# Kernel tuning notes

Hardware: AMD Instinct MI355X
Metric: run time of the kernel (lower is better)

The kernel has to match this reference:

```python
import jax, jax.numpy as jnp
import numpy as np

H = 1024
F = 132

def _lstm_cell(x, h, c, Wih, Whh, bih, bhh):
    # PyTorch LSTMCell: gates ordered i, f, g, o
    gates = x @ Wih.T + bih + h @ Whh.T + bhh  # [B, 4H]
    i, f, g, o = jnp.split(gates, 4, axis=-1)
    i = jax.nn.sigmoid(i)
    f = jax.nn.sigmoid(f)
    g = jnp.tanh(g)
    o = jax.nn.sigmoid(o)
    c_new = f * c + i * g
    h_new = o * jnp.tanh(c_new)
    return h_new, c_new


def setup_inputs() -> dict:
    key = jax.random.key(0)
    ks = jax.random.split(key, 16)
    s = 0.02
    return {
        "initial_seq": jax.random.normal(ks[0], (32, 64, F), dtype=jnp.float32),
        "generate_frames_number": 128,
        "W_ih1": jax.random.normal(ks[1], (4 * H, F), dtype=jnp.float32) * s,
        "W_hh1": jax.random.normal(ks[2], (4 * H, H), dtype=jnp.float32) * s,
        "b_ih1": jax.random.normal(ks[3], (4 * H,), dtype=jnp.float32) * s,
        "b_hh1": jax.random.normal(ks[4], (4 * H,), dtype=jnp.float32) * s,
        "W_ih2": jax.random.normal(ks[5], (4 * H, H), dtype=jnp.float32) * s,
        "W_hh2": jax.random.normal(ks[6], (4 * H, H), dtype=jnp.float32) * s,
        "b_ih2": jax.random.normal(ks[7], (4 * H,), dtype=jnp.float32) * s,
        "b_hh2": jax.random.normal(ks[8], (4 * H,), dtype=jnp.float32) * s,
        "W_ih3": jax.random.normal(ks[9], (4 * H, H), dtype=jnp.float32) * s,
        "W_hh3": jax.random.normal(ks[10], (4 * H, H), dtype=jnp.float32) * s,
        "b_ih3": jax.random.normal(ks[11], (4 * H,), dtype=jnp.float32) * s,
        "b_hh3": jax.random.normal(ks[12], (4 * H,), dtype=jnp.float32) * s,
        "W_dec": jax.random.normal(ks[13], (F, H), dtype=jnp.float32) * s,
        "b_dec": jax.random.normal(ks[14], (F,), dtype=jnp.float32) * s,
    }


def reference(initial_seq, generate_frames_number,
              W_ih1, W_hh1, b_ih1, b_hh1,
              W_ih2, W_hh2, b_ih2, b_hh2,
              W_ih3, W_hh3, b_ih3, b_hh3,
              W_dec, b_dec):
    B = initial_seq.shape[0]
    dt = initial_seq.dtype
    zeros = jnp.zeros((B, H), dtype=dt)
    state0 = (zeros, zeros, zeros, zeros, zeros, zeros)  # h0,h1,h2,c0,c1,c2

    def step(state, in_frame):
        h0, h1, h2, c0, c1, c2 = state
        h0, c0 = _lstm_cell(in_frame, h0, c0, W_ih1, W_hh1, b_ih1, b_hh1)
        h1, c1 = _lstm_cell(h0, h1, c1, W_ih2, W_hh2, b_ih2, b_hh2)
        h2, c2 = _lstm_cell(h1, h2, c2, W_ih3, W_hh3, b_ih3, b_hh3)
        out_frame = h2 @ W_dec.T + b_dec  # [B, F]
        return (h0, h1, h2, c0, c1, c2), out_frame

    # Priming pass over the conditioning sequence (outputs discarded except last)
    def prime_step(carry, in_frame):
        state, _ = carry
        state, out = step(state, in_frame)
        return (state, out), None

    init_frame = jnp.zeros((B, F), dtype=dt)
    xs = jnp.swapaxes(initial_seq, 0, 1)  # [T, B, F]
    (state, cur_frame), _ = jax.lax.scan(prime_step, (state0, init_frame), xs)

    def gen_step(carry, _):
        state, frame = carry
        state, out = step(state, frame)
        return (state, out), out

    _, outs = jax.lax.scan(gen_step, (state, cur_frame), None,
                           length=generate_frames_number)  # [N, B, F]
    return jnp.swapaxes(outs, 0, 1)  # [B, N, F]
```

## Files before the change

### kernel.cpp

```cpp
#include <hip/hip_runtime.h>
#include <stdint.h>

typedef unsigned short u16;
typedef unsigned long long u64;
typedef __attribute__((ext_vector_type(8))) short short8;
typedef __attribute__((ext_vector_type(4))) float f32x4;

#define SZ_BIGW    (4096ull*1024ull*2ull)
#define OFF_WHH1   (0ull)
#define OFF_WIH2   (OFF_WHH1 + SZ_BIGW)
#define OFF_WHH2   (OFF_WIH2 + SZ_BIGW)
#define OFF_WIH3   (OFF_WHH2 + SZ_BIGW)
#define OFF_WHH3   (OFF_WIH3 + SZ_BIGW)
#define OFF_MCOMB  (OFF_WHH3 + SZ_BIGW)
#define OFF_WIH1   (OFF_MCOMB + SZ_BIGW)
#define SZ_WIH1    (4096ull*160ull*2ull)
#define OFF_WDECF  (OFF_WIH1 + SZ_WIH1)
#define SZ_WDECF   (160ull*1024ull*2ull)
#define OFF_WDECB  (OFF_WDECF + SZ_WDECF)
#define SZ_WDECB   (1024ull*160ull*2ull)
#define OFF_XPRIM  (OFF_WDECB + SZ_WDECB)
#define SZ_XPRIM   (64ull*5120ull*2ull)
#define OFF_H2HIST (OFF_XPRIM + SZ_XPRIM)
#define SZ_HSLOT   (32768ull*2ull)
#define SZ_H2HIST  (129ull*SZ_HSLOT)
#define OFF_H0R    (OFF_H2HIST + SZ_H2HIST)
#define SZ_HR      (192ull*SZ_HSLOT)
#define OFF_H1R    (OFF_H0R + SZ_HR)
#define OFF_H2R    (OFF_H1R + SZ_HR)
#define SZ_H2R     (64ull*SZ_HSLOT)
#define OFF_ZEROH  (OFF_H2R + SZ_H2R)
#define OFF_FLAGS  (OFF_ZEROH + SZ_HSLOT)
#define SZ_FLAGS   (4096ull)
#define OFF_BS1    (OFF_FLAGS + SZ_FLAGS)
#define OFF_BS1G   (OFF_BS1 + 16384ull)
#define OFF_BS2    (OFF_BS1G + 16384ull)
#define OFF_BS3    (OFF_BS2 + 16384ull)
#define BLOB_SIZE  (OFF_BS3 + 16384ull)

__device__ unsigned char g_blob[BLOB_SIZE];

#define ZERO_BYTES (SZ_HSLOT + SZ_FLAGS)

__device__ __forceinline__ u16 f2bf(float f) {
  unsigned u = __float_as_uint(f);
  u += 0x7fffu + ((u >> 16) & 1u);
  return (u16)(u >> 16);
}
__device__ __forceinline__ float sigm(float x) { return 1.f / (1.f + __expf(-x)); }
__device__ __forceinline__ float tanh_(float x) {
  x = fminf(fmaxf(x, -40.f), 40.f);
  float e = __expf(2.f * x);
  return (e - 1.f) / (e + 1.f);
}

__global__ __launch_bounds__(256) void k_zero(uint4* p, int n) {
  int i = blockIdx.x * 256 + threadIdx.x;
  for (; i < n; i += gridDim.x * 256) p[i] = make_uint4(0u, 0u, 0u, 0u);
}

__global__ __launch_bounds__(256) void k_swizzle(const float* __restrict__ src, u16* __restrict__ dst,
                                                 int J, int Jsrc, int Kpad, int Ksrc, int srcld,
                                                 int transposed, int perm) {
  int total = J * Kpad;
  int nkc = Kpad >> 3;
  for (int o = blockIdx.x * 256 + threadIdx.x; o < total; o += gridDim.x * 256) {
    int chunk = o >> 7, within = o & 127;
    int nt = chunk / nkc, kc = chunk - nt * nkc;
    int jr = within >> 3, ke = within & 7;
    int j = perm ? ((jr >> 2) * 1024 + nt * 4 + (jr & 3)) : (nt * 16 + jr);
    int k = kc * 8 + ke;
    float v = 0.f;
    if (j < Jsrc && k < Ksrc)
      v = transposed ? src[(size_t)k * srcld + j] : src[(size_t)j * srcld + k];
    dst[o] = f2bf(v);
  }
}

__global__ __launch_bounds__(256) void k_xprim(const float* __restrict__ iseq, u16* __restrict__ dst) {
  int o = blockIdx.x * 256 + threadIdx.x;
  if (o >= 64 * 5120) return;
  int t = o / 5120, rem = o - t * 5120;
  int kc = rem >> 8, b = (rem >> 3) & 31, ke = rem & 7;
  int k = kc * 8 + ke;
  float v = (k < 132) ? iseq[(size_t)b * (64 * 132) + t * 132 + k] : 0.f;
  dst[o] = f2bf(v);
}

__global__ __launch_bounds__(256) void k_bias(const float* bih1, const float* bhh1,
                                              const float* bih2, const float* bhh2,
                                              const float* bih3, const float* bhh3,
                                              const float* __restrict__ Wih1, const float* __restrict__ bdec,
                                              float* bs1, float* bs1g, float* bs2, float* bs3) {
  int j = blockIdx.x * 256 + threadIdx.x;
  if (j >= 4096) return;
  float s1 = bih1[j] + bhh1[j];
  float bc = 0.f;
  const float* wr = Wih1 + (size_t)j * 132;
  for (int f = 0; f < 132; ++f) bc += wr[f] * bdec[f];
  bs1[j] = s1;
  bs1g[j] = s1 + bc;
  bs2[j] = bih2[j] + bhh2[j];
  bs3[j] = bih3[j] + bhh3[j];
}

__global__ __launch_bounds__(256) void k_mcomb(const u16* __restrict__ A, const u16* __restrict__ Bm,
                                               u16* __restrict__ dst) {
  int blk = blockIdx.x;
  int mt = blk & 255, jg = blk >> 8;
  int w = threadIdx.x >> 6, l = threadIdx.x & 63, q = l >> 4, r = l & 15;
  int nt = jg * 4 + w;
  f32x4 acc = {};
  for (int ks = 0; ks < 5; ++ks) {
    short8 a = *(const short8*)(A + ((size_t)mt * 20 + ks * 4 + q) * 128 + r * 8);
    short8 b = *(const short8*)(Bm + ((size_t)nt * 20 + ks * 4 + q) * 128 + r * 8);
    acc = __builtin_amdgcn_mfma_f32_16x16x32_bf16(a, b, acc, 0, 0, 0);
  }
  int kout = nt * 16 + r;
#pragma unroll
  for (int i = 0; i < 4; ++i) {
    int jrow = q * 4 + i;
    dst[(((size_t)mt * 128 + (kout >> 3)) << 7) + jrow * 8 + (kout & 7)] = f2bf(acc[i]);
  }
}


__device__ __forceinline__ void wait_all(unsigned* F, unsigned tgt) {
  if (threadIdx.x < 256) {
    while (__hip_atomic_load(F + threadIdx.x, __ATOMIC_RELAXED, __HIP_MEMORY_SCOPE_AGENT) < tgt)
      __builtin_amdgcn_s_sleep(1);
  }
  __syncthreads();
}

template<bool PRIME>
__device__ __forceinline__ void layer_step(
    const u16* __restrict__ xa,
    const u16* __restrict__ waG,
    const u16* __restrict__ segaL,
    const u16* __restrict__ xb,
    const u16* __restrict__ wbL,
    const u16* __restrict__ stage_g,
    unsigned* waitF, unsigned wtgt,
    const float* __restrict__ bsum, float& creg, u16* __restrict__ hout,
    unsigned* arrF, unsigned aval,
    float (*red)[2][256], u64* hstage, u16* segabuf, int nt)
{
  int tid = threadIdx.x;
  int w = tid >> 6, l = tid & 63, q = l >> 4, r = l & 15;
  f32x4 acc0 = {}, acc1 = {};

  short8 st[4];
  if (stage_g) {
#pragma unroll
    for (int i = 0; i < 4; ++i)
      st[i] = *(const short8*)(stage_g + i * 4096 + tid * 8);
  }

  for (int ks = w; ks < 32; ks += 8) {
    const u16* xp = xb + ks * 1024 + q * 256 + r * 8;
    short8 a0 = *(const short8*)(xp);
    short8 a1 = *(const short8*)(xp + 128);
    short8 bf = *(const short8*)(wbL + ks * 512 + l * 8);
    acc0 = __builtin_amdgcn_mfma_f32_16x16x32_bf16(a0, bf, acc0, 0, 0, 0);
    acc1 = __builtin_amdgcn_mfma_f32_16x16x32_bf16(a1, bf, acc1, 0, 0, 0);
  }

  if (waitF) wait_all(waitF, wtgt);

  if constexpr (PRIME) {
    for (int ks = w; ks < 5; ks += 8) {
      const u16* xp = xa + ks * 1024 + q * 256 + r * 8;
      short8 a0 = *(const short8*)(xp);
      short8 a1 = *(const short8*)(xp + 128);
      short8 bf = *(const short8*)(waG + ((size_t)(ks * 4) << 7) + l * 8);
      acc0 = __builtin_amdgcn_mfma_f32_16x16x32_bf16(a0, bf, acc0, 0, 0, 0);
      acc1 = __builtin_amdgcn_mfma_f32_16x16x32_bf16(a1, bf, acc1, 0, 0, 0);
    }
  } else {
    for (int ks = w; ks < 32; ks += 8) {
      const u16* xp = xa + ks * 1024 + q * 256 + r * 8;
      short8 a0 = *(const short8*)(xp);
      short8 a1 = *(const short8*)(xp + 128);
      short8 bf = *(const short8*)(segaL + ks * 512 + l * 8);
      acc0 = __builtin_amdgcn_mfma_f32_16x16x32_bf16(a0, bf, acc0, 0, 0, 0);
      acc1 = __builtin_amdgcn_mfma_f32_16x16x32_bf16(a1, bf, acc1, 0, 0, 0);
    }
  }

#pragma unroll
  for (int i = 0; i < 4; ++i) { red[w][0][l * 4 + i] = acc0[i]; red[w][1][l * 4 + i] = acc1[i]; }
  __syncthreads();

  if (stage_g) {
#pragma unroll
    for (int i = 0; i < 4; ++i)
      *(short8*)(segabuf + i * 4096 + tid * 8) = st[i];
  }

  if (tid < 128) {
    int b = tid >> 2, hl = tid & 3;
    int mt = b >> 4, row = b & 15;
    int j0 = nt * 4 + hl;
    float g4[4];
#pragma unroll
    for (int g = 0; g < 4; ++g) {
      int col = g * 4 + hl;
      int lidx = ((row >> 2) * 16 + col) * 4 + (row & 3);
      float s = bsum[g * 1024 + j0];
#pragma unroll
      for (int ww = 0; ww < 8; ++ww) s += red[ww][mt][lidx];
      g4[g] = s;
    }
    float iv = sigm(g4[0]), fv = sigm(g4[1]), gv = tanh_(g4[2]), ov = sigm(g4[3]);
    float cn = fv * creg + iv * gv;
    creg = cn;
    ((u16*)hstage)[tid] = f2bf(ov * tanh_(cn));
  }
  __syncthreads();

  if (tid < 64) {
    if (tid < 32) {
      u64 v = hstage[tid];
      u64* dp = (u64*)(hout + ((size_t)(nt >> 1) * 256 + tid * 8 + (nt & 1) * 4));
      __hip_atomic_store(dp, v, __ATOMIC_RELAXED, __HIP_MEMORY_SCOPE_AGENT);
    }
    asm volatile("s_waitcnt vmcnt(0)" ::: "memory");
    if (tid == 0)
      __hip_atomic_store(arrF + nt, aval, __ATOMIC_RELAXED, __HIP_MEMORY_SCOPE_AGENT);
  }
}

__global__ __launch_bounds__(512, 1) void k_rnn(unsigned char* blob) {
  __shared__ u16 whhL[3][16384];
  __shared__ u16 segaL[16384];
  __shared__ float red[8][2][256];
  __shared__ u64 hstage[32];
  const u16* XPRIM = (const u16*)(blob + OFF_XPRIM);
  const u16* tWIH1 = (const u16*)(blob + OFF_WIH1);
  const u16* tMCOMB = (const u16*)(blob + OFF_MCOMB);
  const u16* tWHH1 = (const u16*)(blob + OFF_WHH1);
  const u16* tWIH2 = (const u16*)(blob + OFF_WIH2);
  const u16* tWHH2 = (const u16*)(blob + OFF_WHH2);
  const u16* tWIH3 = (const u16*)(blob + OFF_WIH3);
  const u16* tWHH3 = (const u16*)(blob + OFF_WHH3);
  const float* BS1 = (const float*)(blob + OFF_BS1);
  const float* BS1G = (const float*)(blob + OFF_BS1G);
  const float* BS2 = (const float*)(blob + OFF_BS2);
  const float* BS3 = (const float*)(blob + OFF_BS3);
  u16* H0R = (u16*)(blob + OFF_H0R);
  u16* H1R = (u16*)(blob + OFF_H1R);
  u16* H2R = (u16*)(blob + OFF_H2R);
  u16* H2HIST = (u16*)(blob + OFF_H2HIST);
  const u16* ZEROH = (const u16*)(blob + OFF_ZEROH);
  unsigned* FLAGS = (unsigned*)(blob + OFF_FLAGS);
  unsigned *F1 = FLAGS, *F2 = FLAGS + 256, *F3 = FLAGS + 512;

  int nt = blockIdx.x;
  int tid = threadIdx.x;
  const u16* gWIH1 = tWIH1 + (size_t)nt * 20 * 128;
  const u16* gMCOMB = tMCOMB + (size_t)nt * 16384;
  const u16* gWIH2 = tWIH2 + (size_t)nt * 16384;
  const u16* gWIH3 = tWIH3 + (size_t)nt * 16384;

  {
    const u16* srcs[4] = { tWHH1 + (size_t)nt * 16384, tWHH2 + (size_t)nt * 16384,
                           tWHH3 + (size_t)nt * 16384, gWIH2 };
    u16* dsts[4] = { whhL[0], whhL[1], whhL[2], segaL };
#pragma unroll
    for (int tt = 0; tt < 4; ++tt)
#pragma unroll
      for (int i = 0; i < 4; ++i)
        *(short8*)(dsts[tt] + i * 4096 + tid * 8) = *(const short8*)(srcs[tt] + i * 4096 + tid * 8);
    __syncthreads();
  }

  float c0r = 0.f, c1r = 0.f, c2r = 0.f;

  for (int t = 0; t < 64; ++t) {
    const u16* h0prev = (t == 0) ? ZEROH : H0R + (size_t)(t - 1) * 32768;
    layer_step<true>(XPRIM + t * 5120, gWIH1, nullptr,
                     h0prev, whhL[0], nullptr,
                     F3, (unsigned)t,
                     BS1, c0r, H0R + (size_t)t * 32768,
                     F1, (unsigned)(t + 1), red, hstage, segaL, nt);
    const u16* h1prev = (t == 0) ? ZEROH : H1R + (size_t)(t - 1) * 32768;
    layer_step<false>(H0R + (size_t)t * 32768, nullptr, segaL,
                      h1prev, whhL[1], gWIH3,
                      F1, (unsigned)(t + 1),
                      BS2, c1r, H1R + (size_t)t * 32768,
                      F2, (unsigned)(t + 1), red, hstage, segaL, nt);
    const u16* h2prev = (t == 0) ? ZEROH : H2R + (size_t)(t - 1) * 32768;
    u16* h2out = (t < 63) ? H2R + (size_t)t * 32768 : H2HIST;
    layer_step<false>(H1R + (size_t)t * 32768, nullptr, segaL,
                      h2prev, whhL[2], (t < 63) ? gWIH2 : gMCOMB,
                      F2, (unsigned)(t + 1),
                      BS3, c2r, h2out,
                      F3, (unsigned)(t + 1), red, hstage, segaL, nt);
  }
  for (int t = 64; t < 192; ++t) {
    layer_step<false>(H2HIST + (size_t)(t - 64) * 32768, nullptr, segaL,
                      H0R + (size_t)(t - 1) * 32768, whhL[0], gWIH2,
                      F3, (unsigned)t,
                      BS1G, c0r, H0R + (size_t)t * 32768,
                      F1, (unsigned)(t + 1), red, hstage, segaL, nt);
    layer_step<false>(H0R + (size_t)t * 32768, nullptr, segaL,
                      H1R + (size_t)(t - 1) * 32768, whhL[1], gWIH3,
                      F1, (unsigned)(t + 1),
                      BS2, c1r, H1R + (size_t)t * 32768,
                      F2, (unsigned)(t + 1), red, hstage, segaL, nt);
    layer_step<false>(H1R + (size_t)t * 32768, nullptr, segaL,
                      H2HIST + (size_t)(t - 64) * 32768, whhL[2], gMCOMB,
                      F2, (unsigned)(t + 1),
                      BS3, c2r, H2HIST + (size_t)(t - 63) * 32768,
                      F3, (unsigned)(t + 1), red, hstage, segaL, nt);
  }
}

__global__ __launch_bounds__(256) void k_dec(const u16* __restrict__ h2hist, const u16* __restrict__ Wd,
                                             const float* __restrict__ bdec, float* __restrict__ out) {
  int blk = blockIdx.x;
  int s = blk / 10, nt = blk - s * 10;
  const u16* x = h2hist + (size_t)(s + 1) * 32768;
  int w = threadIdx.x >> 6, l = threadIdx.x & 63, q = l >> 4, r = l & 15;
  f32x4 acc[2] = {};
  for (int ks = w; ks < 32; ks += 4) {
    const u16* xp = x + ks * 1024 + q * 256 + r * 8;
    short8 a0 = *(const short8*)(xp);
    short8 a1 = *(const short8*)(xp + 128);
    short8 bf = *(const short8*)(Wd + (((size_t)nt * 128 + ks * 4) << 7) + l * 8);
    acc[0] = __builtin_amdgcn_mfma_f32_16x16x32_bf16(a0, bf, acc[0], 0, 0, 0);
    acc[1] = __builtin_amdgcn_mfma_f32_16x16x32_bf16(a1, bf, acc[1], 0, 0, 0);
  }
  __shared__ float red[4][2][256];
#pragma unroll
  for (int mt = 0; mt < 2; ++mt)
#pragma unroll
    for (int i = 0; i < 4; ++i) red[w][mt][l * 4 + i] = acc[mt][i];
  __syncthreads();
  for (int pp = threadIdx.x; pp < 512; pp += 256) {
    int b = pp >> 4, fs = pp & 15;
    int mt = b >> 4, row = b & 15;
    int lidx = ((row >> 2) * 16 + fs) * 4 + (row & 3);
    int f = nt * 16 + fs;
    if (f < 132) {
      float v = red[0][mt][lidx] + red[1][mt][lidx] + red[2][mt][lidx] + red[3][mt][lidx] + bdec[f];
      out[(size_t)b * (128 * 132) + s * 132 + f] = v;
    }
  }
}

extern "C" void kernel_launch(void* const* d_in, const int* in_sizes, int n_in,
                              void* d_out, int out_size, void* d_ws, size_t ws_size,
                              hipStream_t stream) {
  unsigned char* blob = nullptr;
  hipGetSymbolAddress((void**)&blob, HIP_SYMBOL(g_blob));

  const float* iseq = (const float*)d_in[0];
  const float* Wih1 = (const float*)d_in[2];
  const float* Whh1 = (const float*)d_in[3];
  const float* bih1 = (const float*)d_in[4];
  const float* bhh1 = (const float*)d_in[5];
  const float* Wih2 = (const float*)d_in[6];
  const float* Whh2 = (const float*)d_in[7];
  const float* bih2 = (const float*)d_in[8];
  const float* bhh2 = (const float*)d_in[9];
  const float* Wih3 = (const float*)d_in[10];
  const float* Whh3 = (const float*)d_in[11];
  const float* bih3 = (const float*)d_in[12];
  const float* bhh3 = (const float*)d_in[13];
  const float* Wdec = (const float*)d_in[14];
  const float* bdec = (const float*)d_in[15];

  u16* tWHH1 = (u16*)(blob + OFF_WHH1);
  u16* tWIH2 = (u16*)(blob + OFF_WIH2);
  u16* tWHH2 = (u16*)(blob + OFF_WHH2);
  u16* tWIH3 = (u16*)(blob + OFF_WIH3);
  u16* tWHH3 = (u16*)(blob + OFF_WHH3);
  u16* tMCOMB = (u16*)(blob + OFF_MCOMB);
  u16* tWIH1 = (u16*)(blob + OFF_WIH1);
  u16* tWDECF = (u16*)(blob + OFF_WDECF);
  u16* tWDECB = (u16*)(blob + OFF_WDECB);
  u16* XPRIM = (u16*)(blob + OFF_XPRIM);
  u16* H2HIST = (u16*)(blob + OFF_H2HIST);
  float* BS1 = (float*)(blob + OFF_BS1);
  float* BS1G = (float*)(blob + OFF_BS1G);
  float* BS2 = (float*)(blob + OFF_BS2);
  float* BS3 = (float*)(blob + OFF_BS3);

  k_zero<<<68, 256, 0, stream>>>((uint4*)(blob + OFF_ZEROH), (int)(ZERO_BYTES / 16));
  k_swizzle<<<2048, 256, 0, stream>>>(Whh1, tWHH1, 4096, 4096, 1024, 1024, 1024, 0, 1);
  k_swizzle<<<2048, 256, 0, stream>>>(Wih2, tWIH2, 4096, 4096, 1024, 1024, 1024, 0, 1);
  k_swizzle<<<2048, 256, 0, stream>>>(Whh2, tWHH2, 4096, 4096, 1024, 1024, 1024, 0, 1);
  k_swizzle<<<2048, 256, 0, stream>>>(Wih3, tWIH3, 4096, 4096, 1024, 1024, 1024, 0, 1);
  k_swizzle<<<2048, 256, 0, stream>>>(Whh3, tWHH3, 4096, 4096, 1024, 1024, 1024, 0, 1);
  k_swizzle<<<2048, 256, 0, stream>>>(Wih1, tWIH1, 4096, 4096, 160, 132, 132, 0, 1);
  k_swizzle<<<512, 256, 0, stream>>>(Wdec, tWDECF, 160, 132, 1024, 1024, 1024, 0, 0);
  k_swizzle<<<512, 256, 0, stream>>>(Wdec, tWDECB, 1024, 1024, 160, 132, 1024, 1, 0);
  k_xprim<<<1280, 256, 0, stream>>>(iseq, XPRIM);
  k_bias<<<16, 256, 0, stream>>>(bih1, bhh1, bih2, bhh2, bih3, bhh3, Wih1, bdec, BS1, BS1G, BS2, BS3);
  k_mcomb<<<4096, 256, 0, stream>>>(tWIH1, tWDECB, tMCOMB);

  {
    void* args[] = { (void*)&blob };
    hipError_t ce = hipLaunchCooperativeKernel((void*)k_rnn, dim3(256), dim3(512), args, 0, stream);
    if (ce != hipSuccess) {
      k_rnn<<<dim3(256), dim3(512), 0, stream>>>(blob);
    }
  }

  k_dec<<<1280, 256, 0, stream>>>(H2HIST, tWDECF, bdec, (float*)d_out);
}
```

Before: 2.369 ms.

## Wavefront-pipeline the three LSTM layers during priming and keep weights in registers

During the 64-step priming phase, the three LSTM layers are now skewed into a diagonal wavefront. Layer k processes timestep b-k in the same iteration, so each iteration needs one grid-wide barrier instead of three sequential ones. All per-block weight slices are moved from LDS into registers (five short8x4 sets plus the decoder-combined matrix). This drops the LDS staging copies of W_ih between layers and lets the cell update for all three layers run on separate thread groups. The cost is much higher register pressure and an extra flag array. The generation phase keeps its three serial barriers per step.

Result: faster. 2.305 ms (-2.7%).

```diff
diff --git a/kernel.cpp b/kernel.cpp
--- a/kernel.cpp
+++ b/kernel.cpp
@@ -133,74 +133,48 @@
   __syncthreads();
 }
 
-template<bool PRIME>
-__device__ __forceinline__ void layer_step(
-    const u16* __restrict__ xa,
-    const u16* __restrict__ waG,
-    const u16* __restrict__ segaL,
-    const u16* __restrict__ xb,
-    const u16* __restrict__ wbL,
-    const u16* __restrict__ stage_g,
+#define MFMA(a, b, c) __builtin_amdgcn_mfma_f32_16x16x32_bf16((a), (b), (c), 0, 0, 0)
+
+template<int LBASE>
+__device__ __forceinline__ void gen_layer(
+    const u16* __restrict__ xa, const short8 (&wA)[4],
+    const u16* __restrict__ xb, const short8 (&wB)[4],
     unsigned* waitF, unsigned wtgt,
     const float* __restrict__ bsum, float& creg, u16* __restrict__ hout,
     unsigned* arrF, unsigned aval,
-    float (*red)[2][256], u64* hstage, u16* segabuf, int nt)
+    float (*red)[2][256], u64* hstage, int nt)
 {
   int tid = threadIdx.x;
   int w = tid >> 6, l = tid & 63, q = l >> 4, r = l & 15;
   f32x4 acc0 = {}, acc1 = {};
 
-  short8 st[4];
-  if (stage_g) {
-#pragma unroll
-    for (int i = 0; i < 4; ++i)
-      st[i] = *(const short8*)(stage_g + i * 4096 + tid * 8);
-  }
-
-  for (int ks = w; ks < 32; ks += 8) {
-    const u16* xp = xb + ks * 1024 + q * 256 + r * 8;
+#pragma unroll
+  for (int i = 0; i < 4; ++i) {
+    const u16* xp = xb + (w + 8 * i) * 1024 + q * 256 + r * 8;
     short8 a0 = *(const short8*)(xp);
     short8 a1 = *(const short8*)(xp + 128);
-    short8 bf = *(const short8*)(wbL + ks * 512 + l * 8);
-    acc0 = __builtin_amdgcn_mfma_f32_16x16x32_bf16(a0, bf, acc0, 0, 0, 0);
-    acc1 = __builtin_amdgcn_mfma_f32_16x16x32_bf16(a1, bf, acc1, 0, 0, 0);
-  }
-
-  if (waitF) wait_all(waitF, wtgt);
-
-  if constexpr (PRIME) {
-    for (int ks = w; ks < 5; ks += 8) {
-      const u16* xp = xa + ks * 1024 + q * 256 + r * 8;
-      short8 a0 = *(const short8*)(xp);
-      short8 a1 = *(const short8*)(xp + 128);
-      short8 bf = *(const short8*)(waG + ((size_t)(ks * 4) << 7) + l * 8);
-      acc0 = __builtin_amdgcn_mfma_f32_16x16x32_bf16(a0, bf, acc0, 0, 0, 0);
-      acc1 = __builtin_amdgcn_mfma_f32_16x16x32_bf16(a1, bf, acc1, 0, 0, 0);
-    }
-  } else {
-    for (int ks = w; ks < 32; ks += 8) {
-      const u16* xp = xa + ks * 1024 + q * 256 + r * 8;
-      short8 a0 = *(const short8*)(xp);
-      short8 a1 = *(const short8*)(xp + 128);
-      short8 bf = *(const short8*)(segaL + ks * 512 + l * 8);
-      acc0 = __builtin_amdgcn_mfma_f32_16x16x32_bf16(a0, bf, acc0, 0, 0, 0);
-      acc1 = __builtin_amdgcn_mfma_f32_16x16x32_bf16(a1, bf, acc1, 0, 0, 0);
-    }
-  }
-
-#pragma unroll
-  for (int i = 0; i < 4; ++i) { red[w][0][l * 4 + i] = acc0[i]; red[w][1][l * 4 + i] = acc1[i]; }
+    acc0 = MFMA(a0, wB[i], acc0);
+    acc1 = MFMA(a1, wB[i], acc1);
+  }
+
+  wait_all(waitF, wtgt);
+
+#pragma unroll
+  for (int i = 0; i < 4; ++i) {
+    const u16* xp = xa + (w + 8 * i) * 1024 + q * 256 + r * 8;
+    short8 a0 = *(const short8*)(xp);
+    short8 a1 = *(const short8*)(xp + 128);
+    acc0 = MFMA(a0, wA[i], acc0);
+    acc1 = MFMA(a1, wA[i], acc1);
+  }
+
+  *(f32x4*)&red[w][0][l * 4] = acc0;
+  *(f32x4*)&red[w][1][l * 4] = acc1;
   __syncthreads();
 
-  if (stage_g) {
-#pragma unroll
-    for (int i = 0; i < 4; ++i)
-      *(short8*)(segabuf + i * 4096 + tid * 8) = st[i];
-  }
-
-  if (tid < 128) {
-    int b = tid >> 2, hl = tid & 3;
-    int mt = b >> 4, row = b & 15;
+  if (tid >= LBASE && tid < LBASE + 128) {
+    int idx = tid - LBASE;
+    int b = idx >> 2, hl = idx & 3, mt = b >> 4, row = b & 15;
     int j0 = nt * 4 + hl;
     float g4[4];
 #pragma unroll
@@ -215,13 +189,13 @@
     float iv = sigm(g4[0]), fv = sigm(g4[1]), gv = tanh_(g4[2]), ov = sigm(g4[3]);
     float cn = fv * creg + iv * gv;
     creg = cn;
-    ((u16*)hstage)[tid] = f2bf(ov * tanh_(cn));
+    ((u16*)hstage)[LBASE + idx] = f2bf(ov * tanh_(cn));
   }
   __syncthreads();
 
   if (tid < 64) {
     if (tid < 32) {
-      u64 v = hstage[tid];
+      u64 v = hstage[(LBASE >> 2) + tid];
       u64* dp = (u64*)(hout + ((size_t)(nt >> 1) * 256 + tid * 8 + (nt & 1) * 4));
       __hip_atomic_store(dp, v, __ATOMIC_RELAXED, __HIP_MEMORY_SCOPE_AGENT);
     }
@@ -232,10 +206,8 @@
 }
 
 __global__ __launch_bounds__(512, 1) void k_rnn(unsigned char* blob) {
-  __shared__ u16 whhL[3][16384];
-  __shared__ u16 segaL[16384];
-  __shared__ float red[8][2][256];
-  __shared__ u64 hstage[32];
+  __shared__ float red3[3][8][2][256];
+  __shared__ u64 hstage[96];
   const u16* XPRIM = (const u16*)(blob + OFF_XPRIM);
   const u16* tWIH1 = (const u16*)(blob + OFF_WIH1);
   const u16* tMCOMB = (const u16*)(blob + OFF_MCOMB);
@@ -254,66 +226,144 @@
   u16* H2HIST = (u16*)(blob + OFF_H2HIST);
   const u16* ZEROH = (const u16*)(blob + OFF_ZEROH);
   unsigned* FLAGS = (unsigned*)(blob + OFF_FLAGS);
-  unsigned *F1 = FLAGS, *F2 = FLAGS + 256, *F3 = FLAGS + 512;
+  unsigned *FP = FLAGS, *F1 = FLAGS + 256, *F2 = FLAGS + 512, *F3 = FLAGS + 768;
 
   int nt = blockIdx.x;
   int tid = threadIdx.x;
-  const u16* gWIH1 = tWIH1 + (size_t)nt * 20 * 128;
-  const u16* gMCOMB = tMCOMB + (size_t)nt * 16384;
-  const u16* gWIH2 = tWIH2 + (size_t)nt * 16384;
-  const u16* gWIH3 = tWIH3 + (size_t)nt * 16384;
-
-  {
-    const u16* srcs[4] = { tWHH1 + (size_t)nt * 16384, tWHH2 + (size_t)nt * 16384,
-                           tWHH3 + (size_t)nt * 16384, gWIH2 };
-    u16* dsts[4] = { whhL[0], whhL[1], whhL[2], segaL };
-#pragma unroll
-    for (int tt = 0; tt < 4; ++tt)
-#pragma unroll
-      for (int i = 0; i < 4; ++i)
-        *(short8*)(dsts[tt] + i * 4096 + tid * 8) = *(const short8*)(srcs[tt] + i * 4096 + tid * 8);
+  int w = tid >> 6, l = tid & 63, q = l >> 4, r = l & 15;
+  int layer = tid >> 7, idx = tid & 127;
+  const float* BSP = (layer == 0) ? BS1 : (layer == 1) ? BS2 : BS3;
+  float creg = 0.f;
+
+  short8 rWhh1[4], rWih2[4], rWhh2[4], rWih3[4], rWhh3[4];
+#pragma unroll
+  for (int i = 0; i < 4; ++i) {
+    size_t off = (size_t)nt * 16384 + (size_t)(w + 8 * i) * 512 + (size_t)l * 8;
+    rWhh1[i] = *(const short8*)(tWHH1 + off);
+    rWih2[i] = *(const short8*)(tWIH2 + off);
+    rWhh2[i] = *(const short8*)(tWHH2 + off);
+    rWih3[i] = *(const short8*)(tWIH3 + off);
+    rWhh3[i] = *(const short8*)(tWHH3 + off);
+  }
+  short8 rWih1 = {};
+  if (w < 5)
+    rWih1 = *(const short8*)(tWIH1 + (size_t)nt * 2560 + (size_t)w * 512 + (size_t)l * 8);
+
+  for (int b = 0; b < 66; ++b) {
+    f32x4 a10 = {}, a11 = {}, a20 = {}, a21 = {}, a30 = {}, a31 = {};
+
+    if (b < 64 && w < 5) {
+      const u16* xp = XPRIM + b * 5120 + w * 1024 + q * 256 + r * 8;
+      short8 x0 = *(const short8*)(xp);
+      short8 x1 = *(const short8*)(xp + 128);
+      a10 = MFMA(x0, rWih1, a10);
+      a11 = MFMA(x1, rWih1, a11);
+    }
+
+    wait_all(FP, (unsigned)b);
+
+    if (b <= 64) {
+      const u16* h0p = (b == 0) ? ZEROH : H0R + (size_t)(b - 1) * 32768;
+#pragma unroll
+      for (int i = 0; i < 4; ++i) {
+        const u16* xp = h0p + (w + 8 * i) * 1024 + q * 256 + r * 8;
+        short8 x0 = *(const short8*)(xp);
+        short8 x1 = *(const short8*)(xp + 128);
+        if (b <= 63) { a10 = MFMA(x0, rWhh1[i], a10); a11 = MFMA(x1, rWhh1[i], a11); }
+        if (b >= 1)  { a20 = MFMA(x0, rWih2[i], a20); a21 = MFMA(x1, rWih2[i], a21); }
+      }
+    }
+    if (b >= 1) {
+      const u16* h1p = (b == 1) ? ZEROH : H1R + (size_t)(b - 2) * 32768;
+#pragma unroll
+      for (int i = 0; i < 4; ++i) {
+        const u16* xp = h1p + (w + 8 * i) * 1024 + q * 256 + r * 8;
+        short8 x0 = *(const short8*)(xp);
+        short8 x1 = *(const short8*)(xp + 128);
+        if (b <= 64) { a20 = MFMA(x0, rWhh2[i], a20); a21 = MFMA(x1, rWhh2[i], a21); }
+        if (b >= 2)  { a30 = MFMA(x0, rWih3[i], a30); a31 = MFMA(x1, rWih3[i], a31); }
+      }
+    }
+    if (b >= 2) {
+      const u16* h2p = (b == 2) ? ZEROH : H2R + (size_t)(b - 3) * 32768;
+#pragma unroll
+      for (int i = 0; i < 4; ++i) {
+        const u16* xp = h2p + (w + 8 * i) * 1024 + q * 256 + r * 8;
+        short8 x0 = *(const short8*)(xp);
+        short8 x1 = *(const short8*)(xp + 128);
+        a30 = MFMA(x0, rWhh3[i], a30);
+        a31 = MFMA(x1, rWhh3[i], a31);
+      }
+    }
+
+    *(f32x4*)&red3[0][w][0][l * 4] = a10;  *(f32x4*)&red3[0][w][1][l * 4] = a11;
+    *(f32x4*)&red3[1][w][0][l * 4] = a20;  *(f32x4*)&red3[1][w][1][l * 4] = a21;
+    *(f32x4*)&red3[2][w][0][l * 4] = a30;  *(f32x4*)&red3[2][w][1][l * 4] = a31;
     __syncthreads();
-  }
-
-  float c0r = 0.f, c1r = 0.f, c2r = 0.f;
-
-  for (int t = 0; t < 64; ++t) {
-    const u16* h0prev = (t == 0) ? ZEROH : H0R + (size_t)(t - 1) * 32768;
-    layer_step<true>(XPRIM + t * 5120, gWIH1, nullptr,
-                     h0prev, whhL[0], nullptr,
-                     F3, (unsigned)t,
-                     BS1, c0r, H0R + (size_t)t * 32768,
-                     F1, (unsigned)(t + 1), red, hstage, segaL, nt);
-    const u16* h1prev = (t == 0) ? ZEROH : H1R + (size_t)(t - 1) * 32768;
-    layer_step<false>(H0R + (size_t)t * 32768, nullptr, segaL,
-                      h1prev, whhL[1], gWIH3,
-                      F1, (unsigned)(t + 1),
-                      BS2, c1r, H1R + (size_t)t * 32768,
-                      F2, (unsigned)(t + 1), red, hstage, segaL, nt);
-    const u16* h2prev = (t == 0) ? ZEROH : H2R + (size_t)(t - 1) * 32768;
-    u16* h2out = (t < 63) ? H2R + (size_t)t * 32768 : H2HIST;
-    layer_step<false>(H1R + (size_t)t * 32768, nullptr, segaL,
-                      h2prev, whhL[2], (t < 63) ? gWIH2 : gMCOMB,
-                      F2, (unsigned)(t + 1),
-                      BS3, c2r, h2out,
-                      F3, (unsigned)(t + 1), red, hstage, segaL, nt);
-  }
+
+    int tb = b - layer;
+    if (tid < 384 && tb >= 0 && tb <= 63) {
+      int bb = idx >> 2, hl = idx & 3, mt = bb >> 4, row = bb & 15;
+      int j0 = nt * 4 + hl;
+      float g4[4];
+#pragma unroll
+      for (int g = 0; g < 4; ++g) {
+        int col = g * 4 + hl;
+        int lidx = ((row >> 2) * 16 + col) * 4 + (row & 3);
+        float s = BSP[g * 1024 + j0];
+#pragma unroll
+        for (int ww = 0; ww < 8; ++ww) s += red3[layer][ww][mt][lidx];
+        g4[g] = s;
+      }
+      float iv = sigm(g4[0]), fv = sigm(g4[1]), gv = tanh_(g4[2]), ov = sigm(g4[3]);
+      float cn = fv * creg + iv * gv;
+      creg = cn;
+      ((u16*)hstage)[tid] = f2bf(ov * tanh_(cn));
+    }
+    __syncthreads();
+
+    if (tid < 64) {
+      if (tid < 32) {
+        size_t doff = (size_t)(nt >> 1) * 256 + (size_t)tid * 8 + (size_t)(nt & 1) * 4;
+        if (b <= 63)
+          __hip_atomic_store((u64*)(H0R + (size_t)b * 32768 + doff), hstage[tid],
+                             __ATOMIC_RELAXED, __HIP_MEMORY_SCOPE_AGENT);
+        if (b >= 1 && b <= 64)
+          __hip_atomic_store((u64*)(H1R + (size_t)(b - 1) * 32768 + doff), hstage[32 + tid],
+                             __ATOMIC_RELAXED, __HIP_MEMORY_SCOPE_AGENT);
+        if (b >= 2) {
+          u16* dst = (b < 65) ? (H2R + (size_t)(b - 2) * 32768) : H2HIST;
+          __hip_atomic_store((u64*)(dst + doff), hstage[64 + tid],
+                             __ATOMIC_RELAXED, __HIP_MEMORY_SCOPE_AGENT);
+        }
+      }
+      asm volatile("s_waitcnt vmcnt(0)" ::: "memory");
+      if (tid == 0)
+        __hip_atomic_store(FP + nt, (unsigned)(b + 1), __ATOMIC_RELAXED, __HIP_MEMORY_SCOPE_AGENT);
+    }
+  }
+
+  short8 rMcomb[4];
+#pragma unroll
+  for (int i = 0; i < 4; ++i)
+    rMcomb[i] = *(const short8*)(tMCOMB + (size_t)nt * 16384 + (size_t)(w + 8 * i) * 512 + (size_t)l * 8);
+
   for (int t = 64; t < 192; ++t) {
-    layer_step<false>(H2HIST + (size_t)(t - 64) * 32768, nullptr, segaL,
-                      H0R + (size_t)(t - 1) * 32768, whhL[0], gWIH2,
-                      F3, (unsigned)t,
-                      BS1G, c0r, H0R + (size_t)t * 32768,
-                      F1, (unsigned)(t + 1), red, hstage, segaL, nt);
-    layer_step<false>(H0R + (size_t)t * 32768, nullptr, segaL,
-                      H1R + (size_t)(t - 1) * 32768, whhL[1], gWIH3,
-                      F1, (unsigned)(t + 1),
-                      BS2, c1r, H1R + (size_t)t * 32768,
-                      F2, (unsigned)(t + 1), red, hstage, segaL, nt);
-    layer_step<false>(H1R + (size_t)t * 32768, nullptr, segaL,
-                      H2HIST + (size_t)(t - 64) * 32768, whhL[2], gMCOMB,
-                      F2, (unsigned)(t + 1),
-                      BS3, c2r, H2HIST + (size_t)(t - 63) * 32768,
-                      F3, (unsigned)(t + 1), red, hstage, segaL, nt);
+    gen_layer<0>(H2HIST + (size_t)(t - 64) * 32768, rMcomb,
+                 H0R + (size_t)(t - 1) * 32768, rWhh1,
+                 (t == 64) ? FP : F3, (t == 64) ? 66u : (unsigned)(t - 64),
+                 BS1G, creg, H0R + (size_t)t * 32768,
+                 F1, (unsigned)(t - 63), red3[0], hstage, nt);
+    gen_layer<128>(H0R + (size_t)t * 32768, rWih2,
+                   H1R + (size_t)(t - 1) * 32768, rWhh2,
+                   F1, (unsigned)(t - 63),
+                   BS2, creg, H1R + (size_t)t * 32768,
+                   F2, (unsigned)(t - 63), red3[0], hstage, nt);
+    gen_layer<256>(H1R + (size_t)t * 32768, rWih3,
+                   H2HIST + (size_t)(t - 64) * 32768, rWhh3,
+                   F2, (unsigned)(t - 63),
+                   BS3, creg, H2HIST + (size_t)(t - 63) * 32768,
+                   F3, (unsigned)(t - 63), red3[0], hstage, nt);
   }
 }
 
```
